# Kernel optimization log

Measured on AMD Instinct MI355X. Metric: run time of the kernel, lower is better.

The kernel has to match this reference:

```python
import jax, jax.numpy as jnp
import numpy as np

CONF_THRESH = 0.25


def setup_inputs() -> dict:
    key = jax.random.key(0)
    # Raw YOLO head output: [batch, n_anchors, 4 box + 1 objectness + 80 classes]
    output = jax.random.uniform(key, (16, 25200, 85), dtype=jnp.float32)
    return {"output": output}


def reference(output):
    # Faithful JAX version of ModelWrapper._process_raw_output fallback path.
    # Torch emits a variable-length [M, 6] tensor; with static shapes we emit
    # the dense [B, N, 6] decoded boxes with below-threshold rows zeroed
    # (equivalent information: masked rows are exactly the dropped ones).
    box_xy = output[..., 0:2]            # [B, N, 2]
    box_wh = output[..., 2:4]            # [B, N, 2]
    box_conf = output[..., 4]            # [B, N]
    box_cls = output[..., 5:]            # [B, N, C]

    half_wh = box_wh * 0.5
    xy_min = box_xy - half_wh            # xmin, ymin
    xy_max = box_xy + half_wh            # xmax, ymax

    max_scores = jnp.max(box_cls, axis=-1)                    # [B, N]
    max_cls_idx = jnp.argmax(box_cls, axis=-1)                # [B, N]
    scores = box_conf * max_scores                            # [B, N]
    mask = scores > CONF_THRESH                               # [B, N]

    boxes = jnp.concatenate(
        [xy_min, xy_max, scores[..., None],
         max_cls_idx.astype(output.dtype)[..., None]], axis=-1)  # [B, N, 6]
    return jnp.where(mask[..., None], boxes, jnp.zeros((), dtype=output.dtype))
```

## Files before the change

### kernel.cpp

```cpp
#include <hip/hip_runtime.h>

#define ROWS_PER_TILE 64
#define THREADS 64
#define ROW_F 85
#define NCLS 80
#define CONF_THRESH 0.25f

#define TILE_F (ROWS_PER_TILE * ROW_F)
#define TILE_V (TILE_F / 4)
#define PER_THREAD 21
#define TAIL_V (TILE_V - PER_THREAD * THREADS)
#define TILES_PER_BLOCK 4

__global__ __launch_bounds__(THREADS) void yolo_post_kernel(
    const float* __restrict__ in, float* __restrict__ out, long long nrows) {
  __shared__ float tile[TILE_F];
  float4* dstv = (float4*)tile;
  const int t = threadIdx.x;

  const long long full_tiles = nrows / ROWS_PER_TILE;
  const long long ntiles = (nrows + ROWS_PER_TILE - 1) / ROWS_PER_TILE;
  long long ti = (long long)blockIdx.x * TILES_PER_BLOCK;
  long long ti_end = ti + TILES_PER_BLOCK;
  if (ti_end > ntiles) ti_end = ntiles;
  if (ti >= ti_end) return;
  long long full_end = ti_end < full_tiles ? ti_end : full_tiles;

  float4 v[PER_THREAD];
  float4 extra;

  if (ti < full_end) {
    {
      const float4* __restrict__ src = (const float4*)(in + ti * TILE_F);
#pragma unroll
      for (int k = 0; k < PER_THREAD; ++k) v[k] = src[t + k * THREADS];
      if (t < TAIL_V) extra = src[PER_THREAD * THREADS + t];
    }
#pragma unroll
    for (int k = 0; k < PER_THREAD; ++k) dstv[t + k * THREADS] = v[k];
    if (t < TAIL_V) dstv[PER_THREAD * THREADS + t] = extra;

    while (ti < full_end) {
      const long long nxt = ti + 1;
      const bool have_next = nxt < full_end;
      if (have_next) {
        const float4* __restrict__ src = (const float4*)(in + nxt * TILE_F);
#pragma unroll
        for (int k = 0; k < PER_THREAD; ++k) v[k] = src[t + k * THREADS];
        if (t < TAIL_V) extra = src[PER_THREAD * THREADS + t];
      }

      const long long r = ti * ROWS_PER_TILE + t;
      const float* row = tile + t * ROW_F;
      float cx = row[0];
      float cy = row[1];
      float hw = row[2] * 0.5f;
      float hh = row[3] * 0.5f;
      float conf = row[4];
      float best = row[5];
      int bidx = 0;
#pragma unroll
      for (int c = 1; c < NCLS; ++c) {
        float x = row[5 + c];
        bool g = x > best;
        best = g ? x : best;
        bidx = g ? c : bidx;
      }
      float score = conf * best;
      bool keep = score > CONF_THRESH;
      float2 o01 = keep ? make_float2(cx - hw, cy - hh) : make_float2(0.f, 0.f);
      float2 o23 = keep ? make_float2(cx + hw, cy + hh) : make_float2(0.f, 0.f);
      float2 o45 = keep ? make_float2(score, (float)bidx) : make_float2(0.f, 0.f);
      float2* op = (float2*)(out + r * 6);
      op[0] = o01;
      op[1] = o23;
      op[2] = o45;

      if (have_next) {
#pragma unroll
        for (int k = 0; k < PER_THREAD; ++k) dstv[t + k * THREADS] = v[k];
        if (t < TAIL_V) dstv[PER_THREAD * THREADS + t] = extra;
      }
      ti = nxt;
    }
  }

  if (ti < ti_end) {
    const long long r = ti * ROWS_PER_TILE + t;
    if (r < nrows) {
      const float* __restrict__ row = in + r * ROW_F;
      float cx = row[0];
      float cy = row[1];
      float hw = row[2] * 0.5f;
      float hh = row[3] * 0.5f;
      float conf = row[4];
      float best = row[5];
      int bidx = 0;
      for (int c = 1; c < NCLS; ++c) {
        float x = row[5 + c];
        bool g = x > best;
        best = g ? x : best;
        bidx = g ? c : bidx;
      }
      float score = conf * best;
      bool keep = score > CONF_THRESH;
      float* op = out + r * 6;
      op[0] = keep ? cx - hw : 0.0f;
      op[1] = keep ? cy - hh : 0.0f;
      op[2] = keep ? cx + hw : 0.0f;
      op[3] = keep ? cy + hh : 0.0f;
      op[4] = keep ? score : 0.0f;
      op[5] = keep ? (float)bidx : 0.0f;
    }
  }
}

extern "C" void kernel_launch(void* const* d_in, const int* in_sizes, int n_in,
                              void* d_out, int out_size, void* d_ws, size_t ws_size,
                              hipStream_t stream) {
  const float* in = (const float*)d_in[0];
  float* out = (float*)d_out;
  const long long nrows = (long long)in_sizes[0] / ROW_F;
  const long long ntiles = (nrows + ROWS_PER_TILE - 1) / ROWS_PER_TILE;
  const int grid = (int)((ntiles + TILES_PER_BLOCK - 1) / TILES_PER_BLOCK);
  yolo_post_kernel<<<grid, THREADS, 0, stream>>>(in, out, nrows);
}
```

Measured before the change: 224.1 us.

## Double-buffer tiles with direct global-to-LDS async loads and more tiles per block

Replaces register-staged global loads followed by LDS stores with `__builtin_amdgcn_global_load_lds` writes straight into a two-slot shared-memory ring. The next tile is prefetched while the current one is reduced. Tiles per block go from 4 to 8. This removes the register round-trip and the VGPR pressure of holding 21 float4 values. In exchange the LDS footprint per block doubles, which can lower occupancy. It also relies on the barrier correctly waiting for the asynchronous LDS writes to complete.

Measured after the change: 206.8 us. 1.08x faster.

```diff
diff --git a/kernel.cpp b/kernel.cpp
--- a/kernel.cpp
+++ b/kernel.cpp
@@ -10,12 +10,14 @@
 #define TILE_V (TILE_F / 4)
 #define PER_THREAD 21
 #define TAIL_V (TILE_V - PER_THREAD * THREADS)
-#define TILES_PER_BLOCK 4
+#define TILES_PER_BLOCK 8
+
+#define GLOBAL_AS __attribute__((address_space(1)))
+#define LDS_AS __attribute__((address_space(3)))
 
 __global__ __launch_bounds__(THREADS) void yolo_post_kernel(
     const float* __restrict__ in, float* __restrict__ out, long long nrows) {
-  __shared__ float tile[TILE_F];
-  float4* dstv = (float4*)tile;
+  __shared__ float tile[2][TILE_F];
   const int t = threadIdx.x;
 
   const long long full_tiles = nrows / ROWS_PER_TILE;
@@ -26,32 +28,30 @@
   if (ti >= ti_end) return;
   long long full_end = ti_end < full_tiles ? ti_end : full_tiles;
 
-  float4 v[PER_THREAD];
-  float4 extra;
+  auto stage = [&](int b, long long tt) {
+    const float* src = in + tt * TILE_F;
+#pragma unroll
+    for (int k = 0; k < PER_THREAD; ++k) {
+      __builtin_amdgcn_global_load_lds(
+          (const GLOBAL_AS void*)(src + (long long)(t + k * THREADS) * 4),
+          (LDS_AS void*)(&tile[b][k * THREADS * 4]), 16, 0, 0);
+    }
+    if (t < TAIL_V) {
+      __builtin_amdgcn_global_load_lds(
+          (const GLOBAL_AS void*)(src + (long long)(t + PER_THREAD * THREADS) * 4),
+          (LDS_AS void*)(&tile[b][PER_THREAD * THREADS * 4]), 16, 0, 0);
+    }
+  };
 
   if (ti < full_end) {
-    {
-      const float4* __restrict__ src = (const float4*)(in + ti * TILE_F);
-#pragma unroll
-      for (int k = 0; k < PER_THREAD; ++k) v[k] = src[t + k * THREADS];
-      if (t < TAIL_V) extra = src[PER_THREAD * THREADS + t];
-    }
-#pragma unroll
-    for (int k = 0; k < PER_THREAD; ++k) dstv[t + k * THREADS] = v[k];
-    if (t < TAIL_V) dstv[PER_THREAD * THREADS + t] = extra;
-
-    while (ti < full_end) {
-      const long long nxt = ti + 1;
-      const bool have_next = nxt < full_end;
-      if (have_next) {
-        const float4* __restrict__ src = (const float4*)(in + nxt * TILE_F);
-#pragma unroll
-        for (int k = 0; k < PER_THREAD; ++k) v[k] = src[t + k * THREADS];
-        if (t < TAIL_V) extra = src[PER_THREAD * THREADS + t];
-      }
+    int cur = 0;
+    stage(0, ti);
+    for (; ti < full_end; ++ti) {
+      __syncthreads();
+      if (ti + 1 < full_end) stage(cur ^ 1, ti + 1);
 
       const long long r = ti * ROWS_PER_TILE + t;
-      const float* row = tile + t * ROW_F;
+      const float* row = &tile[cur][t * ROW_F];
       float cx = row[0];
       float cy = row[1];
       float hw = row[2] * 0.5f;
@@ -76,12 +76,7 @@
       op[1] = o23;
       op[2] = o45;
 
-      if (have_next) {
-#pragma unroll
-        for (int k = 0; k < PER_THREAD; ++k) dstv[t + k * THREADS] = v[k];
-        if (t < TAIL_V) dstv[PER_THREAD * THREADS + t] = extra;
-      }
-      ti = nxt;
+      cur ^= 1;
     }
   }
 
```
